# Kernel tuning notes

Hardware: AMD Instinct MI355X
Metric: run time of the kernel (lower is better)

The kernel has to match this reference:

```python
import jax, jax.numpy as jnp
import numpy as np

NUM_CHUNKS = 8
HEAD_DIM = 128
PROJ = 1024       # projection_size (q)
KV_PROJ = 1024    # kv_projection_size
NEG_INF = -1e30


def _rotate_half(x):
    x1, x2 = jnp.split(x, 2, axis=-1)
    return jnp.concatenate((-x2, x1), axis=-1)


def _apply_rope(x, cos, sin):
    # x: [B, S, H, D]; cos/sin: [B, S, 1, rot_dim] with rot_dim == D here
    return x * cos + _rotate_half(x) * sin


def setup_inputs() -> dict:
    key = jax.random.key(0)
    k1, k2, k3 = jax.random.split(key, 3)
    S, B, H = 8192, 1, 1024
    layernorm_output = jax.random.normal(k1, (S, B, H), dtype=jnp.float32)
    # rotary tables, stored [S, 1, 1, rot_dim] (seq-first, like the torch module)
    inv_freq = 1.0 / (10000.0 ** (jnp.arange(0, HEAD_DIM, 2, dtype=jnp.float32) / HEAD_DIM))
    t = jnp.arange(S, dtype=jnp.float32)
    freqs = jnp.einsum('s,d->sd', t, inv_freq)
    emb = jnp.concatenate((freqs, freqs), axis=-1)  # [S, rot_dim]
    freqs_cos = jnp.cos(emb)[:, None, None, :]
    freqs_sin = jnp.sin(emb)[:, None, None, :]
    qkv_weight = jax.random.normal(k2, (PROJ + 2 * KV_PROJ, H), dtype=jnp.float32) * (H ** -0.5)
    qkv_bias = jax.random.normal(k3, (PROJ + 2 * KV_PROJ,), dtype=jnp.float32) * 0.02
    return {
        'layernorm_output': layernorm_output,
        'freqs_cos': freqs_cos,
        'freqs_sin': freqs_sin,
        'qkv_weight': qkv_weight,
        'qkv_bias': qkv_bias,
    }


def reference(layernorm_output, freqs_cos, freqs_sin, qkv_weight, qkv_bias):
    S, B, H = layernorm_output.shape
    cs = S // NUM_CHUNKS  # chunk size
    scale = HEAD_DIM ** -0.5
    # permute(1,0,2,3): [S,1,1,rot] -> [1,S,1,rot] matching [B, seq, head, dim]
    cos = jnp.transpose(freqs_cos, (1, 0, 2, 3))
    sin = jnp.transpose(freqs_sin, (1, 0, 2, 3))

    outs = []
    k_list, v_list = [], []
    for i in range(NUM_CHUNKS):
        st, ed = i * cs, (i + 1) * cs
        x = layernorm_output[st:ed]                      # [cs, B, H]
        qkv = jnp.einsum('sbh,oh->sbo', x, qkv_weight) + qkv_bias
        def to_bshd(t):
            return jnp.transpose(t.reshape(cs, B, -1, HEAD_DIM), (1, 0, 2, 3))
        q = to_bshd(qkv[..., :PROJ])                     # [B, cs, nH, D]
        k = to_bshd(qkv[..., PROJ:PROJ + KV_PROJ])
        v = to_bshd(qkv[..., PROJ + KV_PROJ:])
        cos_i, sin_i = cos[:, st:ed], sin[:, st:ed]
        q = _apply_rope(q, cos_i, sin_i)
        k = _apply_rope(k, cos_i, sin_i)
        k_list.append(k)
        v_list.append(v)

        K = jnp.concatenate(k_list, axis=1)              # [B, (i+1)*cs, nH, D]
        V = jnp.concatenate(v_list, axis=1)
        scores = jnp.einsum('bqhd,bkhd->bhqk', q, K) * scale
        # causal: query global idx st+r attends keys <= st+r; earlier chunks fully visible
        qidx = st + jnp.arange(cs)
        kidx = jnp.arange((i + 1) * cs)
        mask = kidx[None, :] <= qidx[:, None]            # [cs, (i+1)*cs]
        scores = jnp.where(mask[None, None], scores, NEG_INF)
        p = jax.nn.softmax(scores, axis=-1)
        outs.append(jnp.einsum('bhqk,bkhd->bqhd', p, V))
    return jnp.concatenate(outs, axis=1)                 # [B, S, nH, D]
```

## Files before the change

### kernel.cpp

```cpp
#include <hip/hip_runtime.h>
#include <hip/hip_bf16.h>

typedef float f32x4 __attribute__((ext_vector_type(4)));
typedef __bf16 bf16x8 __attribute__((ext_vector_type(8)));
typedef __bf16 bf16x4 __attribute__((ext_vector_type(4)));

#define S_LEN 8192
#define HIDDEN 1024
#define NH 8
#define HD 128

#define QSCALE (0.08838834764831845f * 1.4426950408889634f)
#define FIXMAX 24.0f

__device__ __forceinline__ void async16(const void* g, void* l) {
  __builtin_amdgcn_global_load_lds(
      (const __attribute__((address_space(1))) char*)g,
      (__attribute__((address_space(3))) char*)l, 16, 0, 0);
}

__global__ void cast_bf16_kernel(const float* __restrict__ in, __bf16* __restrict__ out) {
  int i = (blockIdx.x * blockDim.x + threadIdx.x) * 4;
  float4 v = *(const float4*)(in + i);
  bf16x4 o;
  o[0] = (__bf16)v.x; o[1] = (__bf16)v.y; o[2] = (__bf16)v.z; o[3] = (__bf16)v.w;
  *(bf16x4*)(out + i) = o;
}

__global__ __launch_bounds__(256) void gemm_qkv(
    const __bf16* __restrict__ A, const __bf16* __restrict__ W,
    const float* __restrict__ bias,
    __bf16* __restrict__ Qb, __bf16* __restrict__ Kb, __bf16* __restrict__ Vt)
{
  __shared__ __bf16 As[128 * 32];
  __shared__ __bf16 Bs[128 * 32];
  const int t = threadIdx.x;
  const int lane = t & 63;
  const int w = t >> 6;
  const int wy = w >> 1, wx = w & 1;
  const int quad = lane >> 4, l15 = lane & 15;
  const int m0 = blockIdx.y * 128;
  const int n0 = blockIdx.x * 128;
  f32x4 acc[4][4] = {};
  for (int kt = 0; kt < HIDDEN; kt += 32) {
#pragma unroll
    for (int j = 0; j < 2; ++j) {
      int idx = j * 256 + t;
      int row = idx >> 2, c8 = (idx & 3) * 8;
      async16(A + (size_t)(m0 + row) * HIDDEN + kt + c8, As + idx * 8);
      async16(W + (size_t)(n0 + row) * HIDDEN + kt + c8, Bs + idx * 8);
    }
    __syncthreads();
    bf16x8 af[4], bfr[4];
#pragma unroll
    for (int i = 0; i < 4; ++i)
      af[i] = *(const bf16x8*)(As + (wy * 64 + i * 16 + l15) * 32 + quad * 8);
#pragma unroll
    for (int i = 0; i < 4; ++i)
      bfr[i] = *(const bf16x8*)(Bs + (wx * 64 + i * 16 + l15) * 32 + quad * 8);
#pragma unroll
    for (int mt = 0; mt < 4; ++mt)
#pragma unroll
      for (int nt = 0; nt < 4; ++nt)
        acc[mt][nt] = __builtin_amdgcn_mfma_f32_16x16x32_bf16(af[mt], bfr[nt], acc[mt][nt], 0, 0, 0);
    __syncthreads();
  }
  float bv[4];
  int cols[4];
#pragma unroll
  for (int nt = 0; nt < 4; ++nt) {
    cols[nt] = n0 + wx * 64 + nt * 16 + l15;
    bv[nt] = bias[cols[nt]];
  }
#pragma unroll
  for (int mt = 0; mt < 4; ++mt) {
    int srow_base = m0 + wy * 64 + mt * 16 + quad * 4;
#pragma unroll
    for (int nt = 0; nt < 4; ++nt) {
      int c = cols[nt];
      if (n0 < 1024) {
        int h = c >> 7, d = c & 127;
#pragma unroll
        for (int r = 0; r < 4; ++r)
          Qb[(size_t)h * S_LEN * HD + (size_t)(srow_base + r) * HD + d] =
              (__bf16)(acc[mt][nt][r] + bv[nt]);
      } else if (n0 < 2048) {
        int c2 = c - 1024; int h = c2 >> 7, d = c2 & 127;
#pragma unroll
        for (int r = 0; r < 4; ++r)
          Kb[(size_t)h * S_LEN * HD + (size_t)(srow_base + r) * HD + d] =
              (__bf16)(acc[mt][nt][r] + bv[nt]);
      } else {
        int c2 = c - 2048; int h = c2 >> 7, d = c2 & 127;
        bf16x4 pk;
#pragma unroll
        for (int r = 0; r < 4; ++r) pk[r] = (__bf16)(acc[mt][nt][r] + bv[nt]);
        *(bf16x4*)(Vt + (size_t)h * HD * S_LEN + (size_t)d * S_LEN + srow_base) = pk;
      }
    }
  }
}

__global__ void rope_kernel(__bf16* __restrict__ Qb, __bf16* __restrict__ Kb,
                            const float* __restrict__ fcos, const float* __restrict__ fsin)
{
  int gid = blockIdx.x * blockDim.x + threadIdx.x;
  int d0 = (gid & 15) * 4;
  int h = (gid >> 4) & 7;
  int s = gid >> 7;
  float4 c1 = *(const float4*)(fcos + s * 128 + d0);
  float4 s1 = *(const float4*)(fsin + s * 128 + d0);
  float4 c2 = *(const float4*)(fcos + s * 128 + d0 + 64);
  float4 s2 = *(const float4*)(fsin + s * 128 + d0 + 64);
  size_t base = (size_t)h * S_LEN * HD + (size_t)s * HD + d0;
  bf16x4 qlo = *(const bf16x4*)(Qb + base);
  bf16x4 qhi = *(const bf16x4*)(Qb + base + 64);
  bf16x4 klo = *(const bf16x4*)(Kb + base);
  bf16x4 khi = *(const bf16x4*)(Kb + base + 64);
  bf16x4 qlo_o, qhi_o, klo_o, khi_o;
  const float cc1[4] = {c1.x, c1.y, c1.z, c1.w};
  const float ss1[4] = {s1.x, s1.y, s1.z, s1.w};
  const float cc2[4] = {c2.x, c2.y, c2.z, c2.w};
  const float ss2[4] = {s2.x, s2.y, s2.z, s2.w};
#pragma unroll
  for (int i = 0; i < 4; ++i) {
    float q1 = (float)qlo[i], q2 = (float)qhi[i];
    qlo_o[i] = (__bf16)((q1 * cc1[i] - q2 * ss1[i]) * QSCALE);
    qhi_o[i] = (__bf16)((q2 * cc2[i] + q1 * ss2[i]) * QSCALE);
    float k1 = (float)klo[i], k2 = (float)khi[i];
    klo_o[i] = (__bf16)(k1 * cc1[i] - k2 * ss1[i]);
    khi_o[i] = (__bf16)(k2 * cc2[i] + k1 * ss2[i]);
  }
  *(bf16x4*)(Qb + base)      = qlo_o;
  *(bf16x4*)(Qb + base + 64) = qhi_o;
  *(bf16x4*)(Kb + base)      = klo_o;
  *(bf16x4*)(Kb + base + 64) = khi_o;
}

__global__ __launch_bounds__(256, 3) void attn_kernel(
    const __bf16* __restrict__ Qb, const __bf16* __restrict__ Kb,
    const __bf16* __restrict__ Vt, float* __restrict__ out,
    __bf16* __restrict__ partO, float* __restrict__ partML)
{
  __shared__ __bf16 Ks[2][32 * 128];
  __shared__ __bf16 Vs[2][64 * 64];
  const int t = threadIdx.x;
  const int lane = t & 63, w = t >> 6;
  const int quad = lane >> 4, l15 = lane & 15;
  const int sw = l15 & 7;

  const int id = blockIdx.x;
  const int k = id / 24, r = id % 24;
  int head, qi, piece, j0, j1;
  bool isPartial;
  if (r < 16) { qi = 63 - k; piece = r >> 3; head = r & 7;
                j0 = piece * (2 * qi + 2); j1 = j0 + (2 * qi + 2); isPartial = true; }
  else        { qi = 31 - k; piece = 0; head = r - 16;
                j0 = 0; j1 = 4 * qi + 4; isPartial = false; }
  const int qs = qi * 128;
  const int jmax_w = 4 * qi + w;
  const __bf16* Qh = Qb + (size_t)head * S_LEN * HD;
  const __bf16* Kh = Kb + (size_t)head * S_LEN * HD;
  const __bf16* Vh = Vt + (size_t)head * HD * S_LEN;

  bf16x8 qf[2][4];
#pragma unroll
  for (int qg = 0; qg < 2; ++qg) {
    int qrow = qs + w * 32 + qg * 16 + l15;
#pragma unroll
    for (int dk = 0; dk < 4; ++dk)
      qf[qg][dk] = *(const bf16x8*)(Qh + (size_t)qrow * HD + dk * 32 + quad * 8);
  }

  f32x4 o[2][8] = {};
  float l_loc[2] = {0.f, 0.f};
  const f32x4 FM = {-FIXMAX, -FIXMAX, -FIXMAX, -FIXMAX};

  auto stageK = [&](int j, int sel) {
    const __bf16* Kp = Kh + (size_t)(j * 32) * HD;
    __bf16* Kd = &Ks[sel][0];
#pragma unroll
    for (int li = 0; li < 2; ++li) {
      int slot = li * 256 + t;
      int kr = slot >> 4, cp = slot & 15;
      async16(Kp + (size_t)kr * HD + (cp ^ (kr & 7)) * 8, Kd + slot * 8);
    }
  };
  auto stageV = [&](int j, int sel) {
    const __bf16* Vp = Vh + j * 32;
    __bf16* Vd = &Vs[sel][0];
#pragma unroll
    for (int li = 0; li < 2; ++li) {
      int c = li * 256 + t;
      int rr = c >> 3, sl = c & 7;
      int slu = sl ^ (rr & 7);
      int d = 2 * rr + (slu >> 2);
      async16(Vp + (size_t)d * S_LEN + (slu & 3) * 8, Vd + c * 8);
    }
  };

  stageK(j0, 0);
  stageV(j0, 0);

  for (int j = j0; j < j1; ++j) {
    const int cur = (j - j0) & 1;
    __builtin_amdgcn_s_barrier();
    asm volatile("" ::: "memory");
    const bool pf_next = (j + 1 < j1);
    if (pf_next) {
      stageK(j + 1, cur ^ 1);
      stageV(j + 1, cur ^ 1);
    }
    if (pf_next) asm volatile("s_waitcnt vmcnt(4)" ::: "memory");
    else         asm volatile("s_waitcnt vmcnt(0)" ::: "memory");
    __builtin_amdgcn_sched_barrier(0);
    __builtin_amdgcn_s_barrier();
    asm volatile("" ::: "memory");

    if (j > jmax_w) continue;
    const __bf16* Ksb = &Ks[cur][0];
    const __bf16* Vsb = &Vs[cur][0];

    f32x4 sc[2][2];
#pragma unroll
    for (int mtk = 0; mtk < 2; ++mtk) {
      bf16x8 kf = *(const bf16x8*)(Ksb + (mtk * 16 + l15) * 128 + ((quad ^ sw) * 8));
      sc[0][mtk] = __builtin_amdgcn_mfma_f32_16x16x32_bf16(kf, qf[0][0], FM, 0, 0, 0);
      sc[1][mtk] = __builtin_amdgcn_mfma_f32_16x16x32_bf16(kf, qf[1][0], FM, 0, 0, 0);
    }
#pragma unroll
    for (int dk = 1; dk < 4; ++dk)
#pragma unroll
      for (int mtk = 0; mtk < 2; ++mtk) {
        bf16x8 kf = *(const bf16x8*)(Ksb + (mtk * 16 + l15) * 128 + (((dk * 4 + quad) ^ sw) * 8));
        sc[0][mtk] = __builtin_amdgcn_mfma_f32_16x16x32_bf16(kf, qf[0][dk], sc[0][mtk], 0, 0, 0);
        sc[1][mtk] = __builtin_amdgcn_mfma_f32_16x16x32_bf16(kf, qf[1][dk], sc[1][mtk], 0, 0, 0);
      }

    if (j == jmax_w) {
#pragma unroll
      for (int qg = 0; qg < 2; ++qg)
#pragma unroll
        for (int mtk = 0; mtk < 2; ++mtk)
#pragma unroll
          for (int r2 = 0; r2 < 4; ++r2)
            if (mtk * 16 + quad * 4 + r2 > qg * 16 + l15)
              sc[qg][mtk][r2] = -1e30f;
    }

    bf16x8 pf[2];
#pragma unroll
    for (int qg = 0; qg < 2; ++qg) {
      float p[2][4];
#pragma unroll
      for (int mtk = 0; mtk < 2; ++mtk)
#pragma unroll
        for (int r2 = 0; r2 < 4; ++r2) {
          p[mtk][r2] = __builtin_amdgcn_exp2f(sc[qg][mtk][r2]);
          l_loc[qg] += p[mtk][r2];
        }
      unsigned u0, u1, v0, v1;
      asm("v_cvt_pk_bf16_f32 %0, %1, %2" : "=v"(u0) : "v"(p[0][0]), "v"(p[0][1]));
      asm("v_cvt_pk_bf16_f32 %0, %1, %2" : "=v"(u1) : "v"(p[0][2]), "v"(p[0][3]));
      asm("v_cvt_pk_bf16_f32 %0, %1, %2" : "=v"(v0) : "v"(p[1][0]), "v"(p[1][1]));
      asm("v_cvt_pk_bf16_f32 %0, %1, %2" : "=v"(v1) : "v"(p[1][2]), "v"(p[1][3]));
      asm("v_permlane32_swap_b32 %0, %1" : "+v"(u0), "+v"(v0));
      asm("v_permlane32_swap_b32 %0, %1" : "+v"(u1), "+v"(v1));
      asm("v_permlane16_swap_b32 %0, %1" : "+v"(u0), "+v"(v0));
      asm("v_permlane16_swap_b32 %0, %1" : "+v"(u1), "+v"(v1));
      union { unsigned r4[4]; bf16x8 v8; } pu;
      pu.r4[0] = u0; pu.r4[1] = u1; pu.r4[2] = v0; pu.r4[3] = v1;
      pf[qg] = pu.v8;
    }

#pragma unroll
    for (int dt = 0; dt < 8; ++dt) {
      int d = dt * 16 + l15;
      int rr = d >> 1;
      int slu = ((d & 1) << 2) | quad;
      bf16x8 vf = *(const bf16x8*)(Vsb + rr * 64 + ((slu ^ (rr & 7)) * 8));
      o[0][dt] = __builtin_amdgcn_mfma_f32_16x16x32_bf16(vf, pf[0], o[0][dt], 0, 0, 0);
      o[1][dt] = __builtin_amdgcn_mfma_f32_16x16x32_bf16(vf, pf[1], o[1][dt], 0, 0, 0);
    }
  }

  float inv[2], lfull[2];
#pragma unroll
  for (int qg = 0; qg < 2; ++qg) {
    float lv = l_loc[qg];
    lv += __shfl_xor(lv, 16);
    lv += __shfl_xor(lv, 32);
    lfull[qg] = lv;
    inv[qg] = 1.0f / lv;
  }
  if (!isPartial) {
#pragma unroll
    for (int qg = 0; qg < 2; ++qg) {
      int s = qs + w * 32 + qg * 16 + l15;
#pragma unroll
      for (int dt = 0; dt < 8; ++dt) {
        f32x4 v;
#pragma unroll
        for (int r2 = 0; r2 < 4; ++r2) v[r2] = o[qg][dt][r2] * inv[qg];
        *(f32x4*)(out + (size_t)s * 1024 + head * 128 + dt * 16 + quad * 4) = v;
      }
    }
  } else {
    int u = (qi - 32) * 16 + piece * 8 + head;
    __bf16* Op = partO + (size_t)u * 128 * 128;
    float* mlp = partML + u * 256;
#pragma unroll
    for (int qg = 0; qg < 2; ++qg) {
      int row = w * 32 + qg * 16 + l15;
#pragma unroll
      for (int dt = 0; dt < 8; ++dt) {
        bf16x4 pk;
#pragma unroll
        for (int r2 = 0; r2 < 4; ++r2) pk[r2] = (__bf16)(o[qg][dt][r2] * inv[qg]);
        *(bf16x4*)(Op + row * 128 + dt * 16 + quad * 4) = pk;
      }
    }
    if (quad == 0) {
#pragma unroll
      for (int qg = 0; qg < 2; ++qg)
        mlp[w * 32 + qg * 16 + l15] = lfull[qg];
    }
  }
}

__global__ __launch_bounds__(256) void merge_kernel(
    const __bf16* __restrict__ partO, const float* __restrict__ partML,
    float* __restrict__ out)
{
  int b = blockIdx.x;
  int qi = 32 + (b >> 3), head = b & 7;
  int u0 = (qi - 32) * 16 + head;
  int u1 = u0 + 8;
  int t = threadIdx.x;
  int q = t >> 1, dh = (t & 1) * 64;
  float l0 = partML[u0 * 256 + q];
  float l1 = partML[u1 * 256 + q];
  float inv = 1.0f / (l0 + l1);
  float w0 = l0 * inv, w1 = l1 * inv;
  const __bf16* O0 = partO + ((size_t)u0 * 128 + q) * 128 + dh;
  const __bf16* O1 = partO + ((size_t)u1 * 128 + q) * 128 + dh;
  float* op = out + (size_t)(qi * 128 + q) * 1024 + head * 128 + dh;
#pragma unroll
  for (int d = 0; d < 64; d += 8) {
    bf16x8 a = *(const bf16x8*)(O0 + d);
    bf16x8 c = *(const bf16x8*)(O1 + d);
    float4 r0, r1;
    r0.x = w0 * (float)a[0] + w1 * (float)c[0];
    r0.y = w0 * (float)a[1] + w1 * (float)c[1];
    r0.z = w0 * (float)a[2] + w1 * (float)c[2];
    r0.w = w0 * (float)a[3] + w1 * (float)c[3];
    r1.x = w0 * (float)a[4] + w1 * (float)c[4];
    r1.y = w0 * (float)a[5] + w1 * (float)c[5];
    r1.z = w0 * (float)a[6] + w1 * (float)c[6];
    r1.w = w0 * (float)a[7] + w1 * (float)c[7];
    *(float4*)(op + d) = r0;
    *(float4*)(op + d + 4) = r1;
  }
}

extern "C" void kernel_launch(void* const* d_in, const int* in_sizes, int n_in,
                              void* d_out, int out_size, void* d_ws, size_t ws_size,
                              hipStream_t stream)
{
  const float* x    = (const float*)d_in[0];
  const float* fcos = (const float*)d_in[1];
  const float* fsin = (const float*)d_in[2];
  const float* wq   = (const float*)d_in[3];
  const float* bias = (const float*)d_in[4];
  float* out = (float*)d_out;

  char* ws = (char*)d_ws;
  __bf16* xb = (__bf16*)ws;
  __bf16* wb = (__bf16*)(ws + 16777216);
  __bf16* Qb = (__bf16*)(ws + 23068672);
  __bf16* Kb = (__bf16*)(ws + 39845888);
  __bf16* Vt = (__bf16*)(ws + 56623104);

  __bf16* partO = xb;
  float* partML = (float*)wb;

  cast_bf16_kernel<<<8192, 256, 0, stream>>>(x, xb);
  cast_bf16_kernel<<<3072, 256, 0, stream>>>(wq, wb);
  dim3 gg(24, 64);
  gemm_qkv<<<gg, 256, 0, stream>>>(xb, wb, bias, Qb, Kb, Vt);
  rope_kernel<<<4096, 256, 0, stream>>>(Qb, Kb, fcos, fsin);
  attn_kernel<<<768, 256, 0, stream>>>(Qb, Kb, Vt, out, partO, partML);
  merge_kernel<<<256, 256, 0, stream>>>(partO, partML, out);
}
```

Measured before the change: 349.7 us.

## Split every attention query tile into two KV halves and merge all

The attention work split changes. Before, only the upper 32 query tiles were split into two KV pieces and the rest ran whole. Now every query tile is split into two equal KV halves, giving 1024 uniform blocks. Piece 1 writes its normalized output straight to out, piece 0 writes bf16 partials, and the merge kernel combines them by reading the fp32 out. Occupancy is also raised to 4 blocks per CU. The aim is better load balance and more parallelism, at the cost of more merge traffic and possible register pressure. Empty pieces are guarded with a zero row-sum check.

```diff
diff --git a/kernel.cpp b/kernel.cpp
--- a/kernel.cpp
+++ b/kernel.cpp
@@ -137,7 +137,7 @@
   *(bf16x4*)(Kb + base + 64) = khi_o;
 }
 
-__global__ __launch_bounds__(256, 3) void attn_kernel(
+__global__ __launch_bounds__(256, 4) void attn_kernel(
     const __bf16* __restrict__ Qb, const __bf16* __restrict__ Kb,
     const __bf16* __restrict__ Vt, float* __restrict__ out,
     __bf16* __restrict__ partO, float* __restrict__ partML)
@@ -150,13 +150,11 @@
   const int sw = l15 & 7;
 
   const int id = blockIdx.x;
-  const int k = id / 24, r = id % 24;
-  int head, qi, piece, j0, j1;
-  bool isPartial;
-  if (r < 16) { qi = 63 - k; piece = r >> 3; head = r & 7;
-                j0 = piece * (2 * qi + 2); j1 = j0 + (2 * qi + 2); isPartial = true; }
-  else        { qi = 31 - k; piece = 0; head = r - 16;
-                j0 = 0; j1 = 4 * qi + 4; isPartial = false; }
+  const int qi = 63 - (id >> 4);
+  const int r = id & 15;
+  const int piece = r >> 3, head = r & 7;
+  const int nt2 = 2 * qi + 2;
+  const int j0 = piece * nt2, j1 = j0 + nt2;
   const int qs = qi * 128;
   const int jmax_w = 4 * qi + w;
   const __bf16* Qh = Qb + (size_t)head * S_LEN * HD;
@@ -291,9 +289,10 @@
     lv += __shfl_xor(lv, 16);
     lv += __shfl_xor(lv, 32);
     lfull[qg] = lv;
-    inv[qg] = 1.0f / lv;
-  }
-  if (!isPartial) {
+    inv[qg] = lv > 0.f ? 1.0f / lv : 0.f;
+  }
+  const int u = qi * 8 + head;
+  if (piece == 1) {
 #pragma unroll
     for (int qg = 0; qg < 2; ++qg) {
       int s = qs + w * 32 + qg * 16 + l15;
@@ -306,9 +305,7 @@
       }
     }
   } else {
-    int u = (qi - 32) * 16 + piece * 8 + head;
     __bf16* Op = partO + (size_t)u * 128 * 128;
-    float* mlp = partML + u * 256;
 #pragma unroll
     for (int qg = 0; qg < 2; ++qg) {
       int row = w * 32 + qg * 16 + l15;
@@ -320,11 +317,12 @@
         *(bf16x4*)(Op + row * 128 + dt * 16 + quad * 4) = pk;
       }
     }
-    if (quad == 0) {
-#pragma unroll
-      for (int qg = 0; qg < 2; ++qg)
-        mlp[w * 32 + qg * 16 + l15] = lfull[qg];
-    }
+  }
+  if (quad == 0) {
+    float* mlp = partML + (size_t)u * 512 + piece * 256;
+#pragma unroll
+    for (int qg = 0; qg < 2; ++qg)
+      mlp[w * 32 + qg * 16 + l15] = lfull[qg];
   }
 }
 
@@ -333,31 +331,30 @@
     float* __restrict__ out)
 {
   int b = blockIdx.x;
-  int qi = 32 + (b >> 3), head = b & 7;
-  int u0 = (qi - 32) * 16 + head;
-  int u1 = u0 + 8;
+  int qi = b >> 3, head = b & 7;
+  int u = qi * 8 + head;
   int t = threadIdx.x;
   int q = t >> 1, dh = (t & 1) * 64;
-  float l0 = partML[u0 * 256 + q];
-  float l1 = partML[u1 * 256 + q];
+  float l0 = partML[(size_t)u * 512 + q];
+  float l1 = partML[(size_t)u * 512 + 256 + q];
   float inv = 1.0f / (l0 + l1);
   float w0 = l0 * inv, w1 = l1 * inv;
-  const __bf16* O0 = partO + ((size_t)u0 * 128 + q) * 128 + dh;
-  const __bf16* O1 = partO + ((size_t)u1 * 128 + q) * 128 + dh;
+  const __bf16* O0 = partO + ((size_t)u * 128 + q) * 128 + dh;
   float* op = out + (size_t)(qi * 128 + q) * 1024 + head * 128 + dh;
 #pragma unroll
   for (int d = 0; d < 64; d += 8) {
     bf16x8 a = *(const bf16x8*)(O0 + d);
-    bf16x8 c = *(const bf16x8*)(O1 + d);
+    float4 c0 = *(const float4*)(op + d);
+    float4 c1 = *(const float4*)(op + d + 4);
     float4 r0, r1;
-    r0.x = w0 * (float)a[0] + w1 * (float)c[0];
-    r0.y = w0 * (float)a[1] + w1 * (float)c[1];
-    r0.z = w0 * (float)a[2] + w1 * (float)c[2];
-    r0.w = w0 * (float)a[3] + w1 * (float)c[3];
-    r1.x = w0 * (float)a[4] + w1 * (float)c[4];
-    r1.y = w0 * (float)a[5] + w1 * (float)c[5];
-    r1.z = w0 * (float)a[6] + w1 * (float)c[6];
-    r1.w = w0 * (float)a[7] + w1 * (float)c[7];
+    r0.x = w0 * (float)a[0] + w1 * c0.x;
+    r0.y = w0 * (float)a[1] + w1 * c0.y;
+    r0.z = w0 * (float)a[2] + w1 * c0.z;
+    r0.w = w0 * (float)a[3] + w1 * c0.w;
+    r1.x = w0 * (float)a[4] + w1 * c1.x;
+    r1.y = w0 * (float)a[5] + w1 * c1.y;
+    r1.z = w0 * (float)a[6] + w1 * c1.z;
+    r1.w = w0 * (float)a[7] + w1 * c1.w;
     *(float4*)(op + d) = r0;
     *(float4*)(op + d + 4) = r1;
   }
@@ -389,6 +386,6 @@
   dim3 gg(24, 64);
   gemm_qkv<<<gg, 256, 0, stream>>>(xb, wb, bias, Qb, Kb, Vt);
   rope_kernel<<<4096, 256, 0, stream>>>(Qb, Kb, fcos, fsin);
-  attn_kernel<<<768, 256, 0, stream>>>(Qb, Kb, Vt, out, partO, partML);
-  merge_kernel<<<256, 256, 0, stream>>>(partO, partML, out);
-}
+  attn_kernel<<<1024, 256, 0, stream>>>(Qb, Kb, Vt, out, partO, partML);
+  merge_kernel<<<512, 256, 0, stream>>>(partO, partML, out);
+}
```

Result: slower. 589.6 us (+68.6%).
